# Kernel tuning notes

Measured on AMD Instinct MI355X. Metric: run time of the kernel, lower is better.

## Reference

```python
import jax, jax.numpy as jnp
import numpy as np

B, IN_CH, D, H, W = 2, 4, 8, 224, 224
DS = 4
DIM, HEADS, HEAD_DIM, LAYERS = 256, 8, 32, 4
INNER = HEADS * HEAD_DIM
MLP = 4 * DIM
WS = (4, 8, 8)
SHIFT = (2, 4, 4)
WVOL = WS[0] * WS[1] * WS[2]
Hp, Wp = H // DS, W // DS
NW = (D // WS[0]) * (Hp // WS[1]) * (Wp // WS[2])
NBIAS = (2 * WS[0] - 1) * (2 * WS[1] - 1) * (2 * WS[2] - 1)


def _rel_index():
    c = np.stack(np.meshgrid(np.arange(WS[0]), np.arange(WS[1]), np.arange(WS[2]), indexing='ij')).reshape(3, -1)
    r = (c[:, :, None] - c[:, None, :]).transpose(1, 2, 0)
    r[..., 0] += WS[0] - 1
    r[..., 1] += WS[1] - 1
    r[..., 2] += WS[2] - 1
    return r[..., 0] * (2 * WS[1] - 1) * (2 * WS[2] - 1) + r[..., 1] * (2 * WS[2] - 1) + r[..., 2]

REL_IDX = jnp.asarray(_rel_index())  # (WVOL, WVOL)


def _shift_mask():
    # standard Swin shifted-window attention mask on the post-merge grid
    img = np.zeros((D, Hp, Wp), np.int32)
    cnt = 0
    sl = lambda w, s: (slice(0, -w), slice(-w, -s), slice(-s, None))
    for sd in sl(WS[0], SHIFT[0]):
        for sh in sl(WS[1], SHIFT[1]):
            for sw in sl(WS[2], SHIFT[2]):
                img[sd, sh, sw] = cnt
                cnt += 1
    m = img.reshape(D // WS[0], WS[0], Hp // WS[1], WS[1], Wp // WS[2], WS[2])
    m = m.transpose(0, 2, 4, 1, 3, 5).reshape(NW, WVOL)
    return jnp.asarray(np.where(m[:, None, :] != m[:, :, None], -1e9, 0.0).astype(np.float32))

ATTN_MASK = _shift_mask()  # (NW, WVOL, WVOL)


def layer_norm(x, s, b):
    mu = x.mean(-1, keepdims=True)
    var = x.var(-1, keepdims=True)
    return (x - mu) / jnp.sqrt(var + 1e-5) * s + b


def window_attention(x, qkv_w, out_w, out_b, bias_tab, shifted):
    # x: (B, D, Hp, Wp, C) channel-last
    if shifted:
        x = jnp.roll(x, (-SHIFT[0], -SHIFT[1], -SHIFT[2]), axis=(1, 2, 3))
    xw = x.reshape(B, D // WS[0], WS[0], Hp // WS[1], WS[1], Wp // WS[2], WS[2], DIM)
    xw = xw.transpose(0, 1, 3, 5, 2, 4, 6, 7).reshape(B, NW, WVOL, DIM)
    qkv = xw @ qkv_w  # (B, NW, WVOL, 3*INNER)
    q, k, v = jnp.split(qkv, 3, axis=-1)
    split = lambda t: t.reshape(B, NW, WVOL, HEADS, HEAD_DIM).transpose(0, 1, 3, 2, 4)
    q = split(q) * (HEAD_DIM ** -0.5)
    k, v = split(k), split(v)
    attn = jnp.einsum('bwhid,bwhjd->bwhij', q, k)  # (B, NW, H, WVOL, WVOL)
    bias = bias_tab[REL_IDX].transpose(2, 0, 1)  # (H, WVOL, WVOL)
    attn = attn + bias
    if shifted:
        attn = attn + ATTN_MASK[None, :, None]
    attn = jax.nn.softmax(attn, axis=-1)
    o = jnp.einsum('bwhij,bwhjd->bwhid', attn, v)
    o = o.transpose(0, 1, 3, 2, 4).reshape(B, NW, WVOL, INNER)
    o = o @ out_w + out_b
    o = o.reshape(B, D // WS[0], Hp // WS[1], Wp // WS[2], WS[0], WS[1], WS[2], DIM)
    o = o.transpose(0, 1, 4, 2, 5, 3, 6, 7).reshape(B, D, Hp, Wp, DIM)
    if shifted:
        o = jnp.roll(o, SHIFT, axis=(1, 2, 3))
    return o


def setup_inputs() -> dict:
    key = jax.random.key(0)
    ks = jax.random.split(key, 12)
    s = 0.02
    return {
        'x': jax.random.normal(ks[0], (B, IN_CH, D, H, W), jnp.float32),
        'conv_w': jax.random.normal(ks[1], (DIM, IN_CH, 1, DS, DS), jnp.float32) * s,
        'conv_b': jnp.zeros((DIM,), jnp.float32),
        'ln1_s': jnp.ones((LAYERS, DIM), jnp.float32),
        'ln1_b': jnp.zeros((LAYERS, DIM), jnp.float32),
        'qkv_w': jax.random.normal(ks[2], (LAYERS, DIM, 3 * INNER), jnp.float32) * s,
        'out_w': jax.random.normal(ks[3], (LAYERS, INNER, DIM), jnp.float32) * s,
        'out_b': jnp.zeros((LAYERS, DIM), jnp.float32),
        'bias_tab': jax.random.normal(ks[4], (LAYERS, NBIAS, HEADS), jnp.float32) * s,
        'ln2_s': jnp.ones((LAYERS, DIM), jnp.float32),
        'ln2_b': jnp.zeros((LAYERS, DIM), jnp.float32),
        'fc1_w': jax.random.normal(ks[5], (LAYERS, DIM, MLP), jnp.float32) * s,
        'fc1_b': jnp.zeros((LAYERS, MLP), jnp.float32),
        'fc2_w': jax.random.normal(ks[6], (LAYERS, MLP, DIM), jnp.float32) * s,
        'fc2_b': jnp.zeros((LAYERS, DIM), jnp.float32),
    }


def reference(x, conv_w, conv_b, ln1_s, ln1_b, qkv_w, out_w, out_b, bias_tab, ln2_s, ln2_b, fc1_w, fc1_b, fc2_w, fc2_b):
    # patch merge: Conv3d kernel (1, DS, DS) stride (1, DS, DS)
    y = jax.lax.conv_general_dilated(
        x, conv_w, window_strides=(1, DS, DS), padding='VALID',
        dimension_numbers=('NCDHW', 'OIDHW', 'NCDHW'))
    y = y + conv_b[None, :, None, None, None]
    y = y.transpose(0, 2, 3, 4, 1)  # (B, D, Hp, Wp, DIM) channel-last
    for i in range(LAYERS):
        shifted = (i % 2 == 1)
        y = y + window_attention(layer_norm(y, ln1_s[i], ln1_b[i]),
                                 qkv_w[i], out_w[i], out_b[i], bias_tab[i], shifted)
        h = layer_norm(y, ln2_s[i], ln2_b[i])
        h = jax.nn.gelu(h @ fc1_w[i] + fc1_b[i]) @ fc2_w[i] + fc2_b[i]
        y = y + h
    return y.transpose(0, 4, 1, 2, 3)  # (B, DIM, D, Hp, Wp)
```

## Files before the change

### kernel.cpp

```cpp
#include <hip/hip_runtime.h>

typedef unsigned short ushort_t;
typedef unsigned int   uint_t;

#define NTOK 50176
#define NWIN 98
#define NBIAS 1575

typedef __attribute__((ext_vector_type(8))) short bf16x8;
typedef __attribute__((ext_vector_type(4))) float floatx4;

static __device__ __forceinline__ float lo2f(uint_t u) { return __uint_as_float(u << 16); }
static __device__ __forceinline__ float hi2f(uint_t u) { return __uint_as_float(u & 0xffff0000u); }
static __device__ __forceinline__ ushort_t f2b(float f) {
    union { float f; uint_t u; } v; v.f = f;
    uint_t u = v.u + 0x7fffu + ((v.u >> 16) & 1u);
    return (ushort_t)(u >> 16);
}

__global__ void transpose_w(const float* __restrict__ src, ushort_t* __restrict__ dst,
                            int K, int N) {
    long base = (long)blockIdx.y * K * N;
    int idx = blockIdx.x * 256 + threadIdx.x;
    if (idx < K * N) {
        int k = idx / N, n = idx - k * N;
        dst[base + (long)n * K + k] = f2b(src[base + idx]);
    }
}

__global__ void cast_bf16(const float* __restrict__ src, ushort_t* __restrict__ dst, int n) {
    int i = blockIdx.x * 256 + threadIdx.x;
    if (i < n) dst[i] = f2b(src[i]);
}

__global__ void im2row(const float* __restrict__ X, ushort_t* __restrict__ A) {
    int idx = blockIdx.x * 256 + threadIdx.x;
    int t = idx >> 4;
    int k = idx & 15;
    int ic = k >> 2, kh = k & 3;
    int w = t % 56, h = (t / 56) % 56, d = (t / 3136) % 8, b = t / 25088;
    long xi = (((long)(b * 4 + ic) * 8 + d) * 224 + (h * 4 + kh)) * 224 + w * 4;
    float4 u = *(const float4*)(X + xi);
    ushort_t* ap = A + (long)t * 64 + ic * 16 + kh * 4;
    ap[0] = f2b(u.x); ap[1] = f2b(u.y); ap[2] = f2b(u.z); ap[3] = f2b(u.w);
}

__global__ void ln_kernel(const float* __restrict__ Y, ushort_t* __restrict__ Xn,
                          const float* __restrict__ S, const float* __restrict__ Bb) {
    int wv = threadIdx.x >> 6, lane = threadIdx.x & 63;
    long t = (long)blockIdx.x * 4 + wv;
    const float* y = Y + t * 256;
    float v[4], s = 0.f, s2 = 0.f;
#pragma unroll
    for (int r = 0; r < 4; ++r) { v[r] = y[lane + 64 * r]; s += v[r]; s2 += v[r] * v[r]; }
#pragma unroll
    for (int off = 32; off; off >>= 1) { s += __shfl_xor(s, off, 64); s2 += __shfl_xor(s2, off, 64); }
    float mu = s * (1.f / 256.f);
    float var = s2 * (1.f / 256.f) - mu * mu;
    float rstd = rsqrtf(var + 1e-5f);
#pragma unroll
    for (int r = 0; r < 4; ++r) {
        int c = lane + 64 * r;
        Xn[t * 256 + c] = f2b((v[r] - mu) * rstd * S[c] + Bb[c]);
    }
}

__global__ __launch_bounds__(256, 2) void gemm_bt(
    const ushort_t* __restrict__ A, const ushort_t* __restrict__ BT,
    int M, int N, int K,
    const float* __restrict__ bias, int mode,
    ushort_t* __restrict__ C, float* __restrict__ Y) {
    __shared__ ushort_t As[128 * 32];
    __shared__ ushort_t Bs[128 * 32];
    const int tid = threadIdx.x;
    const int wv = tid >> 6;
    const int lane = tid & 63;
    const int quad = lane >> 4;
    const int l15 = lane & 15;
    const long m0 = (long)blockIdx.x * 128;
    const long n0 = (long)blockIdx.y * 128;
    const int wm = (wv & 1) * 64;
    const int wn = (wv >> 1) * 64;
    const int r_loc = lane >> 2;
    const int k_loc = (lane & 3) * 8;

    floatx4 acc[4][4] = {};

    const ushort_t* Ab = A + m0 * K;
    const ushort_t* Bb = BT + n0 * K;

    for (int kt = 0; kt < K; kt += 32) {
#pragma unroll
        for (int q = 0; q < 2; ++q) {
            int slot = wv * 2 + q;
            int row = slot * 16 + r_loc;
            __builtin_amdgcn_global_load_lds(
                (const __attribute__((address_space(1))) void*)(Ab + (long)row * K + kt + k_loc),
                (__attribute__((address_space(3))) void*)(As + slot * 512), 16, 0, 0);
            __builtin_amdgcn_global_load_lds(
                (const __attribute__((address_space(1))) void*)(Bb + (long)row * K + kt + k_loc),
                (__attribute__((address_space(3))) void*)(Bs + slot * 512), 16, 0, 0);
        }
        __syncthreads();
        bf16x8 af[4], bfr[4];
#pragma unroll
        for (int i = 0; i < 4; ++i) {
            af[i]  = *(const bf16x8*)(As + (wm + i * 16 + l15) * 32 + quad * 8);
            bfr[i] = *(const bf16x8*)(Bs + (wn + i * 16 + l15) * 32 + quad * 8);
        }
#pragma unroll
        for (int mi = 0; mi < 4; ++mi)
#pragma unroll
            for (int ni = 0; ni < 4; ++ni)
                acc[mi][ni] = __builtin_amdgcn_mfma_f32_16x16x32_bf16(af[mi], bfr[ni], acc[mi][ni], 0, 0, 0);
        __syncthreads();
    }

    if (mode == 2) {
#pragma unroll
        for (int mi = 0; mi < 4; ++mi)
#pragma unroll
            for (int ni = 0; ni < 4; ++ni) {
                long col = n0 + wn + ni * 16 + l15;
                float bv = bias[col];
#pragma unroll
                for (int r = 0; r < 4; ++r) {
                    long row = m0 + wm + mi * 16 + quad * 4 + r;
                    Y[row * N + col] += acc[mi][ni][r] + bv;
                }
            }
    } else if (mode == 3) {
#pragma unroll
        for (int mi = 0; mi < 4; ++mi)
#pragma unroll
            for (int ni = 0; ni < 4; ++ni) {
                long col = n0 + wn + ni * 16 + l15;
                float bv = bias[col];
#pragma unroll
                for (int r = 0; r < 4; ++r) {
                    long row = m0 + wm + mi * 16 + quad * 4 + r;
                    Y[row * N + col] = acc[mi][ni][r] + bv;
                }
            }
    } else {
#pragma unroll
        for (int mi = 0; mi < 4; ++mi)
#pragma unroll
            for (int ni = 0; ni < 4; ++ni) {
                long col = n0 + wn + ni * 16 + l15;
                float bv = bias ? bias[col] : 0.f;
#pragma unroll
                for (int r = 0; r < 4; ++r) {
                    long row = m0 + wm + mi * 16 + quad * 4 + r;
                    float v = acc[mi][ni][r] + bv;
                    if (mode == 1) {
                        float x3 = v * v * v;
                        v = 0.5f * v * (1.f + tanhf(0.7978845608028654f * (v + 0.044715f * x3)));
                    }
                    C[row * N + col] = f2b(v);
                }
            }
    }
}

#define PSTRIDE 260
#define VTSTRIDE 264
__global__ __launch_bounds__(256, 2) void attn_mfma(
    const ushort_t* __restrict__ QKV, ushort_t* __restrict__ O,
    const float* __restrict__ BiasTab, int shifted) {
    __shared__ ushort_t Ks[256 * 32];
    __shared__ ushort_t Vt[32 * VTSTRIDE];
    __shared__ ushort_t Pl[4 * 16 * PSTRIDE];
    __shared__ float bias_s[NBIAS];
    __shared__ int tok_s[256];
    __shared__ int reg_s[256];

    const int tid = threadIdx.x;
    const int wv = tid >> 6;
    const int lane = tid & 63;
    const int quad = lane >> 4;
    const int l15 = lane & 15;
    const int wdx = blockIdx.x, hd = blockIdx.y, b = blockIdx.z;
    const int wd = wdx / 49;
    const int wh = (wdx / 7) % 7;
    const int ww = wdx % 7;

    {
        const int t = tid;
        const int di = t >> 6, hi = (t >> 3) & 7, wi = t & 7;
        const int d = wd * 4 + di, h = wh * 8 + hi, w = ww * 8 + wi;
        int d0 = d, h0 = h, w0 = w;
        if (shifted) { d0 = (d + 2) & 7; h0 = (h + 4) % 56; w0 = (w + 4) % 56; }
        const long tok = ((long)((b * 8 + d0) * 56 + h0)) * 56 + w0;
        tok_s[t] = (int)tok;
        if (shifted) {
            int rd = d < 4 ? 0 : (d < 6 ? 1 : 2);
            int rh = h < 48 ? 0 : (h < 52 ? 1 : 2);
            int rw = w < 48 ? 0 : (w < 52 ? 1 : 2);
            reg_s[t] = rd * 9 + rh * 3 + rw;
        } else reg_s[t] = 0;
        const uint4* kp = (const uint4*)(QKV + tok * 768 + 256 + hd * 32);
        const uint4* vp = (const uint4*)(QKV + tok * 768 + 512 + hd * 32);
        uint4* kd = (uint4*)(Ks + t * 32);
#pragma unroll
        for (int p = 0; p < 4; ++p) kd[p] = kp[p];
#pragma unroll
        for (int p = 0; p < 4; ++p) {
            uint4 vvu = vp[p];
            uint_t uu[4] = {vvu.x, vvu.y, vvu.z, vvu.w};
#pragma unroll
            for (int e = 0; e < 4; ++e) {
                int dd = p * 8 + e * 2;
                Vt[dd * VTSTRIDE + t]       = (ushort_t)(uu[e] & 0xffffu);
                Vt[(dd + 1) * VTSTRIDE + t] = (ushort_t)(uu[e] >> 16);
            }
        }
        for (int r = t; r < NBIAS; r += 256) bias_s[r] = BiasTab[r * 8 + hd];
    }
    __syncthreads();

    const float scale = 0.17677669529663687f;
    ushort_t* Pw = Pl + wv * 16 * PSTRIDE;

    for (int rg = 0; rg < 4; ++rg) {
        const int rti = wv * 4 + rg;
        bf16x8 aq;
        {
            int tq = tok_s[rti * 16 + l15];
            const uint4* qp = (const uint4*)(QKV + (long)tq * 768 + hd * 32 + quad * 8);
            union { uint4 u; bf16x8 v; } cv; cv.u = *qp; aq = cv.v;
        }
        int idv[4], ihv[4], iwv4[4], rq[4];
#pragma unroll
        for (int r = 0; r < 4; ++r) {
            int i = rti * 16 + quad * 4 + r;
            idv[r] = i >> 6; ihv[r] = (i >> 3) & 7; iwv4[r] = i & 7;
            rq[r] = reg_s[i];
        }
        floatx4 Sc[16];
#pragma unroll
        for (int nt = 0; nt < 16; ++nt) {
            bf16x8 bk = *(const bf16x8*)(Ks + (nt * 16 + l15) * 32 + quad * 8);
            floatx4 z = {};
            Sc[nt] = __builtin_amdgcn_mfma_f32_16x16x32_bf16(aq, bk, z, 0, 0, 0);
        }
        float m4[4] = {-3e38f, -3e38f, -3e38f, -3e38f};
#pragma unroll
        for (int nt = 0; nt < 16; ++nt) {
            int j = nt * 16 + l15;
            int jd = j >> 6, jh = (j >> 3) & 7, jw = j & 7;
            int rk = reg_s[j];
#pragma unroll
            for (int r = 0; r < 4; ++r) {
                float s = Sc[nt][r] * scale +
                          bias_s[(idv[r] - jd + 3) * 225 + (ihv[r] - jh + 7) * 15 + (iwv4[r] - jw + 7)];
                if (shifted && (rq[r] != rk)) s = -1e9f;
                Sc[nt][r] = s;
                m4[r] = fmaxf(m4[r], s);
            }
        }
#pragma unroll
        for (int r = 0; r < 4; ++r) {
            m4[r] = fmaxf(m4[r], __shfl_xor(m4[r], 1));
            m4[r] = fmaxf(m4[r], __shfl_xor(m4[r], 2));
            m4[r] = fmaxf(m4[r], __shfl_xor(m4[r], 4));
            m4[r] = fmaxf(m4[r], __shfl_xor(m4[r], 8));
        }
        float l4[4] = {0.f, 0.f, 0.f, 0.f};
#pragma unroll
        for (int nt = 0; nt < 16; ++nt)
#pragma unroll
            for (int r = 0; r < 4; ++r) {
                float p = __expf(Sc[nt][r] - m4[r]);
                l4[r] += p;
                Sc[nt][r] = p;
            }
#pragma unroll
        for (int r = 0; r < 4; ++r) {
            l4[r] += __shfl_xor(l4[r], 1);
            l4[r] += __shfl_xor(l4[r], 2);
            l4[r] += __shfl_xor(l4[r], 4);
            l4[r] += __shfl_xor(l4[r], 8);
        }
#pragma unroll
        for (int nt = 0; nt < 16; ++nt)
#pragma unroll
            for (int r = 0; r < 4; ++r)
                Pw[(quad * 4 + r) * PSTRIDE + nt * 16 + l15] = f2b(Sc[nt][r]);
        __builtin_amdgcn_s_waitcnt(0xC07F);
        __builtin_amdgcn_wave_barrier();
        float inv4[4];
#pragma unroll
        for (int r = 0; r < 4; ++r) inv4[r] = 1.f / l4[r];
#pragma unroll
        for (int ct = 0; ct < 2; ++ct) {
            floatx4 oa = {};
#pragma unroll
            for (int kt = 0; kt < 8; ++kt) {
                bf16x8 ap = *(const bf16x8*)(Pw + l15 * PSTRIDE + kt * 32 + quad * 8);
                bf16x8 bv = *(const bf16x8*)(Vt + (ct * 16 + l15) * VTSTRIDE + kt * 32 + quad * 8);
                oa = __builtin_amdgcn_mfma_f32_16x16x32_bf16(ap, bv, oa, 0, 0, 0);
            }
#pragma unroll
            for (int r = 0; r < 4; ++r) {
                int i = rti * 16 + quad * 4 + r;
                long tq = tok_s[i];
                O[tq * 256 + hd * 32 + ct * 16 + l15] = f2b(oa[r] * inv4[r]);
            }
        }
        __builtin_amdgcn_s_waitcnt(0xC07F);
        __builtin_amdgcn_wave_barrier();
    }
}

__global__ void out_permute(const float* __restrict__ Y, float* __restrict__ Out) {
    __shared__ float tile[64][65];
    const int t0 = blockIdx.x * 64;
    const int c0 = blockIdx.y * 64;
    const int tid = threadIdx.x;
    const int a = tid >> 6;
    const int bx = tid & 63;
#pragma unroll
    for (int s8 = 0; s8 < 16; ++s8) {
        int tt = a + s8 * 4;
        tile[tt][bx] = Y[(long)(t0 + tt) * 256 + c0 + bx];
    }
    __syncthreads();
#pragma unroll
    for (int s8 = 0; s8 < 16; ++s8) {
        int cc = a + s8 * 4;
        int tok = t0 + bx;
        int bb = tok / 25088;
        int rem = tok - bb * 25088;
        Out[((long)(bb * 256 + c0 + cc)) * 25088 + rem] = tile[bx][cc];
    }
}

extern "C" void kernel_launch(void* const* d_in, const int* in_sizes, int n_in,
                              void* d_out, int out_size, void* d_ws, size_t ws_size,
                              hipStream_t stream) {
    (void)in_sizes; (void)n_in; (void)out_size; (void)ws_size;
    const float* x        = (const float*)d_in[0];
    const float* conv_w   = (const float*)d_in[1];
    const float* conv_b   = (const float*)d_in[2];
    const float* ln1_s    = (const float*)d_in[3];
    const float* ln1_b    = (const float*)d_in[4];
    const float* qkv_w    = (const float*)d_in[5];
    const float* out_w    = (const float*)d_in[6];
    const float* out_b    = (const float*)d_in[7];
    const float* bias_tab = (const float*)d_in[8];
    const float* ln2_s    = (const float*)d_in[9];
    const float* ln2_b    = (const float*)d_in[10];
    const float* fc1_w    = (const float*)d_in[11];
    const float* fc1_b    = (const float*)d_in[12];
    const float* fc2_w    = (const float*)d_in[13];
    const float* fc2_b    = (const float*)d_in[14];
    float* out = (float*)d_out;

    char* ws = (char*)d_ws;
    float*    y    = (float*)ws;    ws += (size_t)NTOK * 256 * 4;
    ushort_t* big  = (ushort_t*)ws; ws += (size_t)NTOK * 1024 * 2;
    ushort_t* xob  = (ushort_t*)ws; ws += (size_t)NTOK * 256 * 2;
    ushort_t* bt_qkv = (ushort_t*)ws; ws += (size_t)4 * 768 * 256 * 2;
    ushort_t* bt_out = (ushort_t*)ws; ws += (size_t)4 * 256 * 256 * 2;
    ushort_t* bt_fc1 = (ushort_t*)ws; ws += (size_t)4 * 1024 * 256 * 2;
    ushort_t* bt_fc2 = (ushort_t*)ws; ws += (size_t)4 * 256 * 1024 * 2;
    ushort_t* cw_bf  = (ushort_t*)ws; ws += (size_t)256 * 64 * 2;

    transpose_w<<<dim3((256 * 768 + 255) / 256, 4), 256, 0, stream>>>(qkv_w, bt_qkv, 256, 768);
    transpose_w<<<dim3((256 * 256 + 255) / 256, 4), 256, 0, stream>>>(out_w, bt_out, 256, 256);
    transpose_w<<<dim3((256 * 1024 + 255) / 256, 4), 256, 0, stream>>>(fc1_w, bt_fc1, 256, 1024);
    transpose_w<<<dim3((1024 * 256 + 255) / 256, 4), 256, 0, stream>>>(fc2_w, bt_fc2, 1024, 256);

    cast_bf16<<<(256 * 64 + 255) / 256, 256, 0, stream>>>(conv_w, cw_bf, 256 * 64);
    im2row<<<NTOK * 16 / 256, 256, 0, stream>>>(x, big);
    gemm_bt<<<dim3(NTOK / 128, 2), 256, 0, stream>>>(
        big, cw_bf, NTOK, 256, 64, conv_b, 3, nullptr, y);

    for (int i = 0; i < 4; ++i) {
        int sh = i & 1;
        ln_kernel<<<NTOK / 4, 256, 0, stream>>>(y, xob, ln1_s + i * 256, ln1_b + i * 256);
        gemm_bt<<<dim3(NTOK / 128, 6), 256, 0, stream>>>(
            xob, bt_qkv + (size_t)i * 768 * 256, NTOK, 768, 256, nullptr, 0, big, nullptr);
        attn_mfma<<<dim3(NWIN, 8, 2), 256, 0, stream>>>(
            big, xob, bias_tab + (size_t)i * NBIAS * 8, sh);
        gemm_bt<<<dim3(NTOK / 128, 2), 256, 0, stream>>>(
            xob, bt_out + (size_t)i * 256 * 256, NTOK, 256, 256, out_b + i * 256, 2, nullptr, y);
        ln_kernel<<<NTOK / 4, 256, 0, stream>>>(y, xob, ln2_s + i * 256, ln2_b + i * 256);
        gemm_bt<<<dim3(NTOK / 128, 8), 256, 0, stream>>>(
            xob, bt_fc1 + (size_t)i * 1024 * 256, NTOK, 1024, 256, fc1_b + i * 1024, 1, big, nullptr);
        gemm_bt<<<dim3(NTOK / 128, 2), 256, 0, stream>>>(
            big, bt_fc2 + (size_t)i * 256 * 1024, NTOK, 256, 1024, fc2_b + i * 256, 2, nullptr, y);
    }

    out_permute<<<dim3(NTOK / 64, 4), 256, 0, stream>>>(y, out);
}
```

Before: 1.464 ms.

## Precompute dense per-class bias+mask tables and split attention into halves

Adds a setup kernel that expands the relative-position bias and shift mask into dense 256x256 tables per head, one per layer and boundary-window class, pre-scaled by log2(e). The attention kernel now reads these tables from global memory instead of gathering from a shared-memory bias table and comparing region ids. It also switches to exp2, folds the scale into an fma, and processes the P·V product in two halves to shrink the P buffer and allow 3 blocks per CU. The trade is about 37 MB of extra table memory and generation work, plus global bias reads in every attention block.

Measured after the change: 1.424 ms. 1.03x faster.

```diff
diff --git a/kernel.cpp b/kernel.cpp
--- a/kernel.cpp
+++ b/kernel.cpp
@@ -31,6 +31,28 @@
 __global__ void cast_bf16(const float* __restrict__ src, ushort_t* __restrict__ dst, int n) {
     int i = blockIdx.x * 256 + threadIdx.x;
     if (i < n) dst[i] = f2b(src[i]);
+}
+
+__global__ void gen_btab(const float* __restrict__ bias_tab, float* __restrict__ Btab) {
+    int slot = blockIdx.y;
+    int layer, cls;
+    if (slot == 0)      { layer = 0; cls = 0; }
+    else if (slot < 9)  { layer = 1; cls = slot - 1; }
+    else if (slot == 9) { layer = 2; cls = 0; }
+    else                { layer = 3; cls = slot - 10; }
+    int idx = blockIdx.x * 256 + threadIdx.x;
+    int hd = idx >> 16;
+    int ij = idx & 65535;
+    int i = ij >> 8, j = ij & 255;
+    int di = i >> 6, hi = (i >> 3) & 7, wi = i & 7;
+    int dj = j >> 6, hj = (j >> 3) & 7, wj = j & 7;
+    int rel = (di - dj + 3) * 225 + (hi - hj + 7) * 15 + (wi - wj + 7);
+    float v = bias_tab[((long)layer * NBIAS + rel) * 8 + hd];
+    int cd = cls >> 2, ch = (cls >> 1) & 1, cw = cls & 1;
+    int ri = (cd ? (di < 2 ? 1 : 2) : 0) * 9 + (ch ? (hi < 4 ? 1 : 2) : 0) * 3 + (cw ? (wi < 4 ? 1 : 2) : 0);
+    int rj = (cd ? (dj < 2 ? 1 : 2) : 0) * 9 + (ch ? (hj < 4 ? 1 : 2) : 0) * 3 + (cw ? (wj < 4 ? 1 : 2) : 0);
+    if (ri != rj) v = -1e9f;
+    Btab[(long)slot * 524288 + idx] = v * 1.4426950408889634f;
 }
 
 __global__ void im2row(const float* __restrict__ X, ushort_t* __restrict__ A) {
@@ -163,17 +185,15 @@
     }
 }
 
-#define PSTRIDE 260
-#define VTSTRIDE 264
-__global__ __launch_bounds__(256, 2) void attn_mfma(
+#define PSTR 134
+#define VTSTR 266
+__global__ __launch_bounds__(256, 3) void attn_mfma(
     const ushort_t* __restrict__ QKV, ushort_t* __restrict__ O,
-    const float* __restrict__ BiasTab, int shifted) {
+    const float* __restrict__ Btab, int shifted) {
     __shared__ ushort_t Ks[256 * 32];
-    __shared__ ushort_t Vt[32 * VTSTRIDE];
-    __shared__ ushort_t Pl[4 * 16 * PSTRIDE];
-    __shared__ float bias_s[NBIAS];
+    __shared__ ushort_t Vt[32 * VTSTR];
+    __shared__ ushort_t Pl[4 * 16 * PSTR];
     __shared__ int tok_s[256];
-    __shared__ int reg_s[256];
 
     const int tid = threadIdx.x;
     const int wv = tid >> 6;
@@ -185,6 +205,9 @@
     const int wh = (wdx / 7) % 7;
     const int ww = wdx % 7;
 
+    const int cls = shifted ? ((wd << 2) | ((wh == 6) << 1) | (ww == 6)) : 0;
+    const float* bt = Btab + ((long)(cls * 8 + hd)) * 65536;
+
     {
         const int t = tid;
         const int di = t >> 6, hi = (t >> 3) & 7, wi = t & 7;
@@ -193,12 +216,6 @@
         if (shifted) { d0 = (d + 2) & 7; h0 = (h + 4) % 56; w0 = (w + 4) % 56; }
         const long tok = ((long)((b * 8 + d0) * 56 + h0)) * 56 + w0;
         tok_s[t] = (int)tok;
-        if (shifted) {
-            int rd = d < 4 ? 0 : (d < 6 ? 1 : 2);
-            int rh = h < 48 ? 0 : (h < 52 ? 1 : 2);
-            int rw = w < 48 ? 0 : (w < 52 ? 1 : 2);
-            reg_s[t] = rd * 9 + rh * 3 + rw;
-        } else reg_s[t] = 0;
         const uint4* kp = (const uint4*)(QKV + tok * 768 + 256 + hd * 32);
         const uint4* vp = (const uint4*)(QKV + tok * 768 + 512 + hd * 32);
         uint4* kd = (uint4*)(Ks + t * 32);
@@ -211,16 +228,15 @@
 #pragma unroll
             for (int e = 0; e < 4; ++e) {
                 int dd = p * 8 + e * 2;
-                Vt[dd * VTSTRIDE + t]       = (ushort_t)(uu[e] & 0xffffu);
-                Vt[(dd + 1) * VTSTRIDE + t] = (ushort_t)(uu[e] >> 16);
-            }
-        }
-        for (int r = t; r < NBIAS; r += 256) bias_s[r] = BiasTab[r * 8 + hd];
+                Vt[dd * VTSTR + t]       = (ushort_t)(uu[e] & 0xffffu);
+                Vt[(dd + 1) * VTSTR + t] = (ushort_t)(uu[e] >> 16);
+            }
+        }
     }
     __syncthreads();
 
-    const float scale = 0.17677669529663687f;
-    ushort_t* Pw = Pl + wv * 16 * PSTRIDE;
+    const float scale = 0.17677669529663687f * 1.4426950408889634f;
+    ushort_t* Pw = Pl + wv * 16 * PSTR;
 
     for (int rg = 0; rg < 4; ++rg) {
         const int rti = wv * 4 + rg;
@@ -230,33 +246,33 @@
             const uint4* qp = (const uint4*)(QKV + (long)tq * 768 + hd * 32 + quad * 8);
             union { uint4 u; bf16x8 v; } cv; cv.u = *qp; aq = cv.v;
         }
-        int idv[4], ihv[4], iwv4[4], rq[4];
-#pragma unroll
-        for (int r = 0; r < 4; ++r) {
-            int i = rti * 16 + quad * 4 + r;
-            idv[r] = i >> 6; ihv[r] = (i >> 3) & 7; iwv4[r] = i & 7;
-            rq[r] = reg_s[i];
-        }
+        const float* bp = bt + (long)(rti * 16 + quad * 4) * 256 + l15;
         floatx4 Sc[16];
-#pragma unroll
-        for (int nt = 0; nt < 16; ++nt) {
-            bf16x8 bk = *(const bf16x8*)(Ks + (nt * 16 + l15) * 32 + quad * 8);
-            floatx4 z = {};
-            Sc[nt] = __builtin_amdgcn_mfma_f32_16x16x32_bf16(aq, bk, z, 0, 0, 0);
-        }
         float m4[4] = {-3e38f, -3e38f, -3e38f, -3e38f};
 #pragma unroll
-        for (int nt = 0; nt < 16; ++nt) {
-            int j = nt * 16 + l15;
-            int jd = j >> 6, jh = (j >> 3) & 7, jw = j & 7;
-            int rk = reg_s[j];
-#pragma unroll
-            for (int r = 0; r < 4; ++r) {
-                float s = Sc[nt][r] * scale +
-                          bias_s[(idv[r] - jd + 3) * 225 + (ihv[r] - jh + 7) * 15 + (iwv4[r] - jw + 7)];
-                if (shifted && (rq[r] != rk)) s = -1e9f;
-                Sc[nt][r] = s;
-                m4[r] = fmaxf(m4[r], s);
+        for (int hf = 0; hf < 2; ++hf) {
+            float bb[8][4];
+#pragma unroll
+            for (int n8 = 0; n8 < 8; ++n8)
+#pragma unroll
+                for (int r = 0; r < 4; ++r)
+                    bb[n8][r] = bp[r * 256 + (hf * 8 + n8) * 16];
+#pragma unroll
+            for (int n8 = 0; n8 < 8; ++n8) {
+                const int nt = hf * 8 + n8;
+                bf16x8 bk = *(const bf16x8*)(Ks + (nt * 16 + l15) * 32 + quad * 8);
+                floatx4 z = {};
+                Sc[nt] = __builtin_amdgcn_mfma_f32_16x16x32_bf16(aq, bk, z, 0, 0, 0);
+            }
+#pragma unroll
+            for (int n8 = 0; n8 < 8; ++n8) {
+                const int nt = hf * 8 + n8;
+#pragma unroll
+                for (int r = 0; r < 4; ++r) {
+                    float s = fmaf(Sc[nt][r], scale, bb[n8][r]);
+                    Sc[nt][r] = s;
+                    m4[r] = fmaxf(m4[r], s);
+                }
             }
         }
 #pragma unroll
@@ -271,7 +287,7 @@
         for (int nt = 0; nt < 16; ++nt)
 #pragma unroll
             for (int r = 0; r < 4; ++r) {
-                float p = __expf(Sc[nt][r] - m4[r]);
+                float p = __builtin_amdgcn_exp2f(Sc[nt][r] - m4[r]);
                 l4[r] += p;
                 Sc[nt][r] = p;
             }
@@ -282,34 +298,39 @@
             l4[r] += __shfl_xor(l4[r], 4);
             l4[r] += __shfl_xor(l4[r], 8);
         }
-#pragma unroll
-        for (int nt = 0; nt < 16; ++nt)
-#pragma unroll
-            for (int r = 0; r < 4; ++r)
-                Pw[(quad * 4 + r) * PSTRIDE + nt * 16 + l15] = f2b(Sc[nt][r]);
-        __builtin_amdgcn_s_waitcnt(0xC07F);
-        __builtin_amdgcn_wave_barrier();
         float inv4[4];
 #pragma unroll
         for (int r = 0; r < 4; ++r) inv4[r] = 1.f / l4[r];
-#pragma unroll
-        for (int ct = 0; ct < 2; ++ct) {
-            floatx4 oa = {};
-#pragma unroll
-            for (int kt = 0; kt < 8; ++kt) {
-                bf16x8 ap = *(const bf16x8*)(Pw + l15 * PSTRIDE + kt * 32 + quad * 8);
-                bf16x8 bv = *(const bf16x8*)(Vt + (ct * 16 + l15) * VTSTRIDE + kt * 32 + quad * 8);
-                oa = __builtin_amdgcn_mfma_f32_16x16x32_bf16(ap, bv, oa, 0, 0, 0);
-            }
+
+        floatx4 oa[2] = {};
+#pragma unroll
+        for (int hf = 0; hf < 2; ++hf) {
+#pragma unroll
+            for (int n8 = 0; n8 < 8; ++n8)
+#pragma unroll
+                for (int r = 0; r < 4; ++r)
+                    Pw[(quad * 4 + r) * PSTR + n8 * 16 + l15] = f2b(Sc[hf * 8 + n8][r]);
+            __builtin_amdgcn_s_waitcnt(0xC07F);
+            __builtin_amdgcn_wave_barrier();
+#pragma unroll
+            for (int ct = 0; ct < 2; ++ct)
+#pragma unroll
+                for (int kt = 0; kt < 4; ++kt) {
+                    bf16x8 ap = *(const bf16x8*)(Pw + l15 * PSTR + kt * 32 + quad * 8);
+                    bf16x8 bv = *(const bf16x8*)(Vt + (ct * 16 + l15) * VTSTR + hf * 128 + kt * 32 + quad * 8);
+                    oa[ct] = __builtin_amdgcn_mfma_f32_16x16x32_bf16(ap, bv, oa[ct], 0, 0, 0);
+                }
+            __builtin_amdgcn_s_waitcnt(0xC07F);
+            __builtin_amdgcn_wave_barrier();
+        }
+#pragma unroll
+        for (int ct = 0; ct < 2; ++ct)
 #pragma unroll
             for (int r = 0; r < 4; ++r) {
                 int i = rti * 16 + quad * 4 + r;
                 long tq = tok_s[i];
-                O[tq * 256 + hd * 32 + ct * 16 + l15] = f2b(oa[r] * inv4[r]);
-            }
-        }
-        __builtin_amdgcn_s_waitcnt(0xC07F);
-        __builtin_amdgcn_wave_barrier();
+                O[tq * 256 + hd * 32 + ct * 16 + l15] = f2b(oa[ct][r] * inv4[r]);
+            }
     }
 }
 
@@ -366,24 +387,27 @@
     ushort_t* bt_fc1 = (ushort_t*)ws; ws += (size_t)4 * 1024 * 256 * 2;
     ushort_t* bt_fc2 = (ushort_t*)ws; ws += (size_t)4 * 256 * 1024 * 2;
     ushort_t* cw_bf  = (ushort_t*)ws; ws += (size_t)256 * 64 * 2;
+    float*    btab   = (float*)ws;  ws += (size_t)18 * 524288 * 4;
 
     transpose_w<<<dim3((256 * 768 + 255) / 256, 4), 256, 0, stream>>>(qkv_w, bt_qkv, 256, 768);
     transpose_w<<<dim3((256 * 256 + 255) / 256, 4), 256, 0, stream>>>(out_w, bt_out, 256, 256);
     transpose_w<<<dim3((256 * 1024 + 255) / 256, 4), 256, 0, stream>>>(fc1_w, bt_fc1, 256, 1024);
     transpose_w<<<dim3((1024 * 256 + 255) / 256, 4), 256, 0, stream>>>(fc2_w, bt_fc2, 1024, 256);
+    gen_btab<<<dim3(2048, 18), 256, 0, stream>>>(bias_tab, btab);
 
     cast_bf16<<<(256 * 64 + 255) / 256, 256, 0, stream>>>(conv_w, cw_bf, 256 * 64);
     im2row<<<NTOK * 16 / 256, 256, 0, stream>>>(x, big);
     gemm_bt<<<dim3(NTOK / 128, 2), 256, 0, stream>>>(
         big, cw_bf, NTOK, 256, 64, conv_b, 3, nullptr, y);
 
+    static const int base_slot[4] = {0, 1, 9, 10};
     for (int i = 0; i < 4; ++i) {
         int sh = i & 1;
         ln_kernel<<<NTOK / 4, 256, 0, stream>>>(y, xob, ln1_s + i * 256, ln1_b + i * 256);
         gemm_bt<<<dim3(NTOK / 128, 6), 256, 0, stream>>>(
             xob, bt_qkv + (size_t)i * 768 * 256, NTOK, 768, 256, nullptr, 0, big, nullptr);
         attn_mfma<<<dim3(NWIN, 8, 2), 256, 0, stream>>>(
-            big, xob, bias_tab + (size_t)i * NBIAS * 8, sh);
+            big, xob, btab + (size_t)base_slot[i] * 524288, sh);
         gemm_bt<<<dim3(NTOK / 128, 2), 256, 0, stream>>>(
             xob, bt_out + (size_t)i * 256 * 256, NTOK, 256, 256, out_b + i * 256, 2, nullptr, y);
         ln_kernel<<<NTOK / 4, 256, 0, stream>>>(y, xob, ln2_s + i * 256, ln2_b + i * 256);
```
